# Kernel optimization log

Measured on AMD Instinct MI355X. Metric: run time of the kernel, lower is better.

Reference implementation:

```python
import jax, jax.numpy as jnp
import numpy as np

B, K, I, H = 128, 512, 512, 512  # batch, seq_len, input_dim, hidden_dim


def setup_inputs() -> dict:
    key = jax.random.key(0)
    k1, k2, k3, k4, k5 = jax.random.split(key, 5)
    s_i = 1.0 / np.sqrt(H)
    return {
        "visual_seq": jax.random.normal(k1, (B, K, I), dtype=jnp.float32),
        # PyTorch GRU layout: gates stacked [r, z, n] along first dim
        "W_ih": jax.random.uniform(k2, (3 * H, I), minval=-s_i, maxval=s_i, dtype=jnp.float32),
        "W_hh": jax.random.uniform(k3, (3 * H, H), minval=-s_i, maxval=s_i, dtype=jnp.float32),
        "b_ih": jax.random.uniform(k4, (3 * H,), minval=-s_i, maxval=s_i, dtype=jnp.float32),
        "b_hh": jax.random.uniform(k5, (3 * H,), minval=-s_i, maxval=s_i, dtype=jnp.float32),
    }


def reference(visual_seq, W_ih, W_hh, b_ih, b_hh):
    # Fused single-layer GRU over all K steps (equivalent to the per-frame
    # torch loop with zero-initialized hidden state).
    Bs, Ks, _ = visual_seq.shape
    Hs = W_hh.shape[1]
    # Precompute input-gate projections for all timesteps: (K, B, 3H)
    x_gates = jnp.einsum('bki,gi->kbg', visual_seq, W_ih) + b_ih

    def step(h, xg):
        hg = h @ W_hh.T + b_hh                      # (B, 3H)
        xr, xz, xn = jnp.split(xg, 3, axis=-1)
        hr, hz, hn = jnp.split(hg, 3, axis=-1)
        r = jax.nn.sigmoid(xr + hr)
        z = jax.nn.sigmoid(xz + hz)
        n = jnp.tanh(xn + r * hn)
        h_new = (1.0 - z) * n + z * h
        return h_new, None

    h0 = jnp.zeros((Bs, Hs), dtype=visual_seq.dtype)
    h_final, _ = jax.lax.scan(step, h0, x_gates)
    return h_final  # (B, H) == h[-1] in the torch code
```

## Files before the change

kernel.cpp:

```cpp
#include <hip/hip_runtime.h>
#include <hip/hip_bf16.h>


#define CH 32
#define XG_BYTES (CH * 128 * 1536 * 4)
#define HB_BYTES (2 * 128 * 512 * 2)
#define HSTATE_BYTES (128 * 512 * 4)
#define CNT_STRIDE 16
#define CNT_BYTES (512 * 4 * CNT_STRIDE * 4)

typedef float  floatx4 __attribute__((ext_vector_type(4)));
typedef short  shortx8 __attribute__((ext_vector_type(8)));

__device__ __forceinline__ unsigned short f2bf(float f) {
    unsigned int u = __float_as_uint(f);
    u = (u + 0x7FFFu + ((u >> 16) & 1u)) >> 16;
    return (unsigned short)u;
}

__global__ __launch_bounds__(256, 1)
void gru_fused(const float* __restrict__ vis, const float* __restrict__ Wih,
               const float* __restrict__ bih, const float* __restrict__ Whh,
               const float* __restrict__ bhh,
               const float* __restrict__ xgR, float* __restrict__ xgW,
               unsigned short* __restrict__ hb, float* __restrict__ hstate,
               unsigned int* __restrict__ cnt, float* __restrict__ out,
               int kg0, int gemm_kg0, int do_rec, int do_gemm) {
    __shared__ unsigned short Ast[64][40];
    __shared__ unsigned short Bst[64][40];

    const int bx = blockIdx.x;
    const int t = threadIdx.x;
    const int wave = t >> 6, lane = t & 63, quad = lane >> 4, l16 = lane & 15;

    if (do_rec && bx < 64) {
        const int ug = bx & 15, bg = bx >> 4;
        const int u0 = ug * 32, b0 = bg * 32;
        const int mt = wave & 1, u16 = wave >> 1;
        const int b_base = b0 + mt * 16 + quad * 4;
        const int u = u0 + u16 * 16 + l16;

        shortx8 w[3][16];
        #pragma unroll
        for (int g = 0; g < 3; ++g) {
            #pragma unroll
            for (int kt = 0; kt < 16; ++kt) {
                const float* p = Whh + ((size_t)(g * 512 + u)) * 512 + kt * 32 + quad * 8;
                float4 a = *(const float4*)p;
                float4 b = *(const float4*)(p + 4);
                shortx8 v;
                v[0] = (short)f2bf(a.x); v[1] = (short)f2bf(a.y);
                v[2] = (short)f2bf(a.z); v[3] = (short)f2bf(a.w);
                v[4] = (short)f2bf(b.x); v[5] = (short)f2bf(b.y);
                v[6] = (short)f2bf(b.z); v[7] = (short)f2bf(b.w);
                w[g][kt] = v;
            }
        }
        const float bhr = bhh[u], bhz = bhh[512 + u], bhn = bhh[1024 + u];

        float hp[4];
        if (kg0 == 0) {
            hp[0] = hp[1] = hp[2] = hp[3] = 0.f;
        } else {
            #pragma unroll
            for (int reg = 0; reg < 4; ++reg) hp[reg] = hstate[(size_t)(b_base + reg) * 512 + u];
        }

        for (int s = 0; s < CH; ++s) {
            const int kg = kg0 + s;
            float xr[4], xz[4], xn[4];
            #pragma unroll
            for (int reg = 0; reg < 4; ++reg) {
                const float* xgp = xgR + ((size_t)s * 128 + b_base + reg) * 1536 + u;
                xr[reg] = xgp[0]; xz[reg] = xgp[512]; xn[reg] = xgp[1024];
            }

            union { unsigned long long u8[2]; shortx8 v; } af[16];
            if (kg > 0) {
                const unsigned int* fp = cnt + ((size_t)(kg - 1) * 4 + bg) * CNT_STRIDE;
                while (__hip_atomic_load(fp, __ATOMIC_RELAXED, __HIP_MEMORY_SCOPE_AGENT) < 16u)
                    __builtin_amdgcn_s_sleep(1);
                const unsigned short* hsrc = hb + (size_t)((kg - 1) & 1) * (128 * 512)
                                                + (size_t)(b0 + mt * 16 + l16) * 512 + quad * 8;
                #pragma unroll
                for (int kt = 0; kt < 16; ++kt) {
                    af[kt].u8[0] = __hip_atomic_load((const unsigned long long*)(hsrc + kt * 32),
                                                     __ATOMIC_RELAXED, __HIP_MEMORY_SCOPE_AGENT);
                    af[kt].u8[1] = __hip_atomic_load((const unsigned long long*)(hsrc + kt * 32 + 4),
                                                     __ATOMIC_RELAXED, __HIP_MEMORY_SCOPE_AGENT);
                }
            } else {
                #pragma unroll
                for (int kt = 0; kt < 16; ++kt) { af[kt].u8[0] = 0ull; af[kt].u8[1] = 0ull; }
            }

            floatx4 aR = {0,0,0,0}, aZ = {0,0,0,0}, aN = {0,0,0,0};
            #pragma unroll
            for (int kt = 0; kt < 16; ++kt) {
                aR = __builtin_amdgcn_mfma_f32_16x16x32_bf16(af[kt].v, w[0][kt], aR, 0, 0, 0);
                aZ = __builtin_amdgcn_mfma_f32_16x16x32_bf16(af[kt].v, w[1][kt], aZ, 0, 0, 0);
                aN = __builtin_amdgcn_mfma_f32_16x16x32_bf16(af[kt].v, w[2][kt], aN, 0, 0, 0);
            }

            unsigned short* hdst = hb + (size_t)(kg & 1) * (128 * 512);
            #pragma unroll
            for (int reg = 0; reg < 4; ++reg) {
                const float r = 1.f / (1.f + __expf(-(xr[reg] + aR[reg] + bhr)));
                const float z = 1.f / (1.f + __expf(-(xz[reg] + aZ[reg] + bhz)));
                const float n = tanhf(xn[reg] + r * (aN[reg] + bhn));
                const float h = (1.f - z) * n + z * hp[reg];
                hp[reg] = h;
                const float h_odd = __shfl_xor(h, 1);
                if (!(lane & 1)) {
                    unsigned int pk = (unsigned int)f2bf(h) | ((unsigned int)f2bf(h_odd) << 16);
                    __hip_atomic_store((unsigned int*)(hdst + (size_t)(b_base + reg) * 512 + u),
                                       pk, __ATOMIC_RELAXED, __HIP_MEMORY_SCOPE_AGENT);
                }
                if (kg == 511) out[(size_t)(b_base + reg) * 512 + u] = h;
            }
            __syncthreads();
            if (t == 0)
                __hip_atomic_fetch_add(cnt + ((size_t)kg * 4 + bg) * CNT_STRIDE, 1u,
                                       __ATOMIC_RELAXED, __HIP_MEMORY_SCOPE_AGENT);
        }

        #pragma unroll
        for (int reg = 0; reg < 4; ++reg)
            hstate[(size_t)(b_base + reg) * 512 + u] = hp[reg];
        return;
    }

    if (!do_gemm) return;
    const int NG = do_rec ? 192 : 256;
    const int gid = do_rec ? bx - 64 : bx;

    for (int T = gid; T < 1536; T += NG) {
        const int g0 = (T % 24) * 64;
        const int m0 = (T / 24) * 64;
        const int kc = m0 >> 7;
        const int b0 = m0 & 127;
        const int kg = gemm_kg0 + kc;

        floatx4 acc[4] = {{0,0,0,0},{0,0,0,0},{0,0,0,0},{0,0,0,0}};

        for (int ki = 0; ki < 16; ++ki) {
            const int i0 = ki * 32;
            #pragma unroll
            for (int rep = 0; rep < 2; ++rep) {
                const int r = (t >> 3) + rep * 32;
                const int c = (t & 7) * 4;
                float4 av = *(const float4*)(vis + ((size_t)(b0 + r) * 512 + kg) * 512 + i0 + c);
                ushort4 ab; ab.x = f2bf(av.x); ab.y = f2bf(av.y); ab.z = f2bf(av.z); ab.w = f2bf(av.w);
                *(ushort4*)&Ast[r][c] = ab;
                float4 bv = *(const float4*)(Wih + (size_t)(g0 + r) * 512 + i0 + c);
                ushort4 bb; bb.x = f2bf(bv.x); bb.y = f2bf(bv.y); bb.z = f2bf(bv.z); bb.w = f2bf(bv.w);
                *(ushort4*)&Bst[r][c] = bb;
            }
            __syncthreads();
            shortx8 afr = *(const shortx8*)(&Ast[wave * 16 + l16][quad * 8]);
            #pragma unroll
            for (int nb = 0; nb < 4; ++nb) {
                shortx8 bfr = *(const shortx8*)(&Bst[nb * 16 + l16][quad * 8]);
                acc[nb] = __builtin_amdgcn_mfma_f32_16x16x32_bf16(afr, bfr, acc[nb], 0, 0, 0);
            }
            __syncthreads();
        }
        #pragma unroll
        for (int nb = 0; nb < 4; ++nb) {
            const int g = g0 + nb * 16 + l16;
            const float bi = bih[g];
            #pragma unroll
            for (int reg = 0; reg < 4; ++reg) {
                const int m = m0 + wave * 16 + quad * 4 + reg;
                xgW[(size_t)m * 1536 + g] = acc[nb][reg] + bi;
            }
        }
    }
}

extern "C" void kernel_launch(void* const* d_in, const int* in_sizes, int n_in,
                              void* d_out, int out_size, void* d_ws, size_t ws_size,
                              hipStream_t stream) {
    const float* vis = (const float*)d_in[0];
    const float* Wih = (const float*)d_in[1];
    const float* Whh = (const float*)d_in[2];
    const float* bih = (const float*)d_in[3];
    const float* bhh = (const float*)d_in[4];
    float* out = (float*)d_out;

    char* ws = (char*)d_ws;
    float* xg0 = (float*)ws;
    float* xg1 = (float*)(ws + XG_BYTES);
    unsigned short* hb = (unsigned short*)(ws + 2 * XG_BYTES);
    float* hstate = (float*)(ws + 2 * XG_BYTES + HB_BYTES);
    unsigned int* cnt = (unsigned int*)(ws + 2 * XG_BYTES + HB_BYTES + HSTATE_BYTES);

    hipMemsetAsync(cnt, 0, CNT_BYTES, stream);

    float* bufs[2] = {xg0, xg1};

    gru_fused<<<256, 256, 0, stream>>>(vis, Wih, bih, Whh, bhh,
                                       xg0, xg0, hb, hstate, cnt, out,
                                       0, 0, 0, 1);
    for (int i = 0; i < 16; ++i) {
        gru_fused<<<256, 256, 0, stream>>>(vis, Wih, bih, Whh, bhh,
                                           bufs[i & 1], bufs[(i + 1) & 1],
                                           hb, hstate, cnt, out,
                                           i * CH, (i + 1) * CH, 1, (i < 15) ? 1 : 0);
    }
}
```

Measured before the change: 3.657 ms.

## Replace per-step block barrier and counter with per-wave monotonic flags

Each wave now publishes its progress by storing a step number into its own flag instead of the block doing __syncthreads plus a shared atomic counter increment. Consumers poll the 32 relevant producer flags across lanes and use a ballot to wait until all have reached the current step. The recurrent-state loads become inline dwordx4 loads with sc0 sc1 cache bits in place of paired 64-bit atomic loads. The aim is to cut the block-wide barrier and atomic contention from the serial recurrence critical path. In exchange, correctness now depends on the hand-written waitcnt before each flag store for ordering, and the flag memory layout and initialisation change.

Result: faster. 3.046 ms (-16.7%).

```diff
diff --git a/kernel.cpp b/kernel.cpp
--- a/kernel.cpp
+++ b/kernel.cpp
@@ -66,6 +66,11 @@
             for (int reg = 0; reg < 4; ++reg) hp[reg] = hstate[(size_t)(b_base + reg) * 512 + u];
         }
 
+        unsigned int* const myflag =
+            cnt + ((size_t)((bg * 2 + mt) * 32 + (ug * 2 + u16))) * CNT_STRIDE;
+        const unsigned int* const pollflag =
+            cnt + ((size_t)((bg * 2 + mt) * 32 + (lane & 31))) * CNT_STRIDE;
+
         for (int s = 0; s < CH; ++s) {
             const int kg = kg0 + s;
             float xr[4], xz[4], xn[4];
@@ -77,18 +82,23 @@
 
             union { unsigned long long u8[2]; shortx8 v; } af[16];
             if (kg > 0) {
-                const unsigned int* fp = cnt + ((size_t)(kg - 1) * 4 + bg) * CNT_STRIDE;
-                while (__hip_atomic_load(fp, __ATOMIC_RELAXED, __HIP_MEMORY_SCOPE_AGENT) < 16u)
+                for (;;) {
+                    unsigned int v = __hip_atomic_load(pollflag, __ATOMIC_RELAXED,
+                                                       __HIP_MEMORY_SCOPE_AGENT);
+                    if (__ballot(v < (unsigned int)kg) == 0ull) break;
                     __builtin_amdgcn_s_sleep(1);
+                }
                 const unsigned short* hsrc = hb + (size_t)((kg - 1) & 1) * (128 * 512)
                                                 + (size_t)(b0 + mt * 16 + l16) * 512 + quad * 8;
                 #pragma unroll
                 for (int kt = 0; kt < 16; ++kt) {
-                    af[kt].u8[0] = __hip_atomic_load((const unsigned long long*)(hsrc + kt * 32),
-                                                     __ATOMIC_RELAXED, __HIP_MEMORY_SCOPE_AGENT);
-                    af[kt].u8[1] = __hip_atomic_load((const unsigned long long*)(hsrc + kt * 32 + 4),
-                                                     __ATOMIC_RELAXED, __HIP_MEMORY_SCOPE_AGENT);
+                    asm volatile("global_load_dwordx4 %0, %1, off sc0 sc1"
+                                 : "=v"(af[kt].v)
+                                 : "v"(hsrc + kt * 32)
+                                 : "memory");
                 }
+                asm volatile("s_waitcnt vmcnt(0)" ::: "memory");
+                __builtin_amdgcn_sched_barrier(0);
             } else {
                 #pragma unroll
                 for (int kt = 0; kt < 16; ++kt) { af[kt].u8[0] = 0ull; af[kt].u8[1] = 0ull; }
@@ -118,10 +128,11 @@
                 }
                 if (kg == 511) out[(size_t)(b_base + reg) * 512 + u] = h;
             }
-            __syncthreads();
-            if (t == 0)
-                __hip_atomic_fetch_add(cnt + ((size_t)kg * 4 + bg) * CNT_STRIDE, 1u,
-                                       __ATOMIC_RELAXED, __HIP_MEMORY_SCOPE_AGENT);
+            asm volatile("s_waitcnt vmcnt(0)" ::: "memory");
+            __builtin_amdgcn_sched_barrier(0);
+            if (lane == 0)
+                __hip_atomic_store(myflag, (unsigned int)(kg + 1), __ATOMIC_RELAXED,
+                                   __HIP_MEMORY_SCOPE_AGENT);
         }
 
         #pragma unroll
```

## Replace counter-based step sync with tagged hidden-state words and split GEMM/recurrence kernels

Applied to the files above, without the earlier changes.

Each hidden-state pair is now stored together with a step tag in a 64-bit word. Consumers poll the tags directly instead of waiting on a per-step block counter that needed a __syncthreads plus an atomic add. W_hh is kept in swizzled LDS rather than registers, and tanh is computed from exp. The input-projection GEMM moves to a separate kernel that runs between recurrence chunks of 64 steps, so it no longer overlaps with the recurrence; the single xg buffer and the extra launches serialize the two phases.

Measured after the change: 4.459 ms. 21.9% more time.

```diff
diff --git a/kernel.cpp b/kernel.cpp
--- a/kernel.cpp
+++ b/kernel.cpp
@@ -1,140 +1,162 @@
 #include <hip/hip_runtime.h>
-#include <hip/hip_bf16.h>
-
-
-#define CH 32
+
+
+#define CH 64
 #define XG_BYTES (CH * 128 * 1536 * 4)
-#define HB_BYTES (2 * 128 * 512 * 2)
-#define HSTATE_BYTES (128 * 512 * 4)
-#define CNT_STRIDE 16
-#define CNT_BYTES (512 * 4 * CNT_STRIDE * 4)
+#define HBT_BYTES (2 * 128 * 256 * 8)
 
 typedef float  floatx4 __attribute__((ext_vector_type(4)));
 typedef short  shortx8 __attribute__((ext_vector_type(8)));
+typedef unsigned int uintx4 __attribute__((ext_vector_type(4)));
 
 __device__ __forceinline__ unsigned short f2bf(float f) {
-    unsigned int u = __float_as_uint(f);
-    u = (u + 0x7FFFu + ((u >> 16) & 1u)) >> 16;
-    return (unsigned short)u;
+    unsigned int uu = __float_as_uint(f);
+    uu = (uu + 0x7FFFu + ((uu >> 16) & 1u)) >> 16;
+    return (unsigned short)uu;
 }
 
 __global__ __launch_bounds__(256, 1)
-void gru_fused(const float* __restrict__ vis, const float* __restrict__ Wih,
-               const float* __restrict__ bih, const float* __restrict__ Whh,
-               const float* __restrict__ bhh,
-               const float* __restrict__ xgR, float* __restrict__ xgW,
-               unsigned short* __restrict__ hb, float* __restrict__ hstate,
-               unsigned int* __restrict__ cnt, float* __restrict__ out,
-               int kg0, int gemm_kg0, int do_rec, int do_gemm) {
+void gru_rec(const float* __restrict__ xgR, const float* __restrict__ Whh,
+             const float* __restrict__ bhh,
+             unsigned long long* __restrict__ hbt, float* __restrict__ out,
+             int kg0) {
+    __shared__ unsigned short Wl[96 * 512];
+
+    const int bx = blockIdx.x, t = threadIdx.x;
+    const int wave = t >> 6, lane = t & 63, quad = lane >> 4, l16 = lane & 15;
+    const int ug = bx & 15, bg = bx >> 4;
+    const int u0 = ug * 32, b0 = bg * 32;
+    const int mt = wave & 1, u16 = wave >> 1;
+    const int b_base = b0 + mt * 16 + quad * 4;
+    const int u = u0 + u16 * 16 + l16;
+    const int rrow = b0 + mt * 16 + l16;
+
+    for (int i = t; i < 96 * 128; i += 256) {
+        const int r = i >> 7, cq = i & 127;
+        const int g = r >> 5, lu = r & 31;
+        const float* p = Whh + ((size_t)(g * 512 + u0 + lu)) * 512 + cq * 4;
+        float4 vv = *(const float4*)p;
+        ushort4 b4;
+        b4.x = f2bf(vv.x); b4.y = f2bf(vv.y); b4.z = f2bf(vv.z); b4.w = f2bf(vv.w);
+        *(ushort4*)&Wl[r * 512 + ((cq * 4) ^ ((r & 7) << 3))] = b4;
+    }
+    __syncthreads();
+
+    const float bhr = bhh[u], bhz = bhh[512 + u], bhn = bhh[1024 + u];
+    const int rb = u16 * 16 + l16, xrw = (rb & 7) << 3;
+
+    float hp[4];
+    if (kg0 == 0) {
+        hp[0] = hp[1] = hp[2] = hp[3] = 0.f;
+    } else {
+        #pragma unroll
+        for (int reg = 0; reg < 4; ++reg) hp[reg] = out[(size_t)(b_base + reg) * 512 + u];
+    }
+
+    for (int s = 0; s < CH; ++s) {
+        const int kg = kg0 + s;
+        float xr[4], xz[4], xn[4];
+        #pragma unroll
+        for (int reg = 0; reg < 4; ++reg) {
+            const float* xgp = xgR + ((size_t)s * 128 + b_base + reg) * 1536 + u;
+            xr[reg] = xgp[0]; xz[reg] = xgp[512]; xn[reg] = xgp[1024];
+        }
+
+        union { unsigned int d[4]; shortx8 v; } af[16];
+        if (kg > 0) {
+            const unsigned int expv = (unsigned int)(kg - 1);
+            const size_t pbase = (size_t)((kg - 1) & 1) * 32768;
+            const unsigned long long* sp = hbt + pbase + (size_t)rrow * 256
+                                              + ((lane & 31) >> 1) * 16 + (lane & 1) * 8;
+            for (;;) {
+                unsigned int tg = (unsigned int)(__hip_atomic_load(sp, __ATOMIC_RELAXED,
+                                                 __HIP_MEMORY_SCOPE_AGENT) >> 32);
+                if (__ballot(tg != expv) == 0ull) break;
+                __builtin_amdgcn_s_sleep(1);
+            }
+            const unsigned long long* hbp = hbt + pbase + (size_t)rrow * 256 + quad * 4;
+            union { uintx4 v; unsigned int d[4]; } Tq[32];
+            for (;;) {
+                #define LDT(i, OFF) asm volatile("global_load_dwordx4 %0, %1, off offset:" OFF " sc0 sc1" \
+                        : "=v"(Tq[i].v) : "v"(hbp) : "memory");
+                LDT(0,"0")     LDT(1,"16")    LDT(2,"128")   LDT(3,"144")
+                LDT(4,"256")   LDT(5,"272")   LDT(6,"384")   LDT(7,"400")
+                LDT(8,"512")   LDT(9,"528")   LDT(10,"640")  LDT(11,"656")
+                LDT(12,"768")  LDT(13,"784")  LDT(14,"896")  LDT(15,"912")
+                LDT(16,"1024") LDT(17,"1040") LDT(18,"1152") LDT(19,"1168")
+                LDT(20,"1280") LDT(21,"1296") LDT(22,"1408") LDT(23,"1424")
+                LDT(24,"1536") LDT(25,"1552") LDT(26,"1664") LDT(27,"1680")
+                LDT(28,"1792") LDT(29,"1808") LDT(30,"1920") LDT(31,"1936")
+                #undef LDT
+                asm volatile("s_waitcnt vmcnt(0)" ::: "memory");
+                __builtin_amdgcn_sched_barrier(0);
+                unsigned int err = 0u;
+                #pragma unroll
+                for (int i = 0; i < 32; ++i)
+                    err |= (Tq[i].d[1] ^ expv) | (Tq[i].d[3] ^ expv);
+                if (__ballot(err != 0u) == 0ull) break;
+                __builtin_amdgcn_s_sleep(1);
+            }
+            #pragma unroll
+            for (int kt = 0; kt < 16; ++kt) {
+                af[kt].d[0] = Tq[2 * kt].d[0];     af[kt].d[1] = Tq[2 * kt].d[2];
+                af[kt].d[2] = Tq[2 * kt + 1].d[0]; af[kt].d[3] = Tq[2 * kt + 1].d[2];
+            }
+        } else {
+            #pragma unroll
+            for (int kt = 0; kt < 16; ++kt) {
+                af[kt].d[0] = 0u; af[kt].d[1] = 0u; af[kt].d[2] = 0u; af[kt].d[3] = 0u;
+            }
+        }
+
+        floatx4 aR = {0,0,0,0}, aZ = {0,0,0,0}, aN = {0,0,0,0};
+        #pragma unroll
+        for (int kt = 0; kt < 16; ++kt) {
+            const int co = (kt * 32 + quad * 8) ^ xrw;
+            shortx8 bR = *(const shortx8*)&Wl[(size_t)rb * 512 + co];
+            shortx8 bZ = *(const shortx8*)&Wl[(size_t)(32 + rb) * 512 + co];
+            shortx8 bN = *(const shortx8*)&Wl[(size_t)(64 + rb) * 512 + co];
+            aR = __builtin_amdgcn_mfma_f32_16x16x32_bf16(af[kt].v, bR, aR, 0, 0, 0);
+            aZ = __builtin_amdgcn_mfma_f32_16x16x32_bf16(af[kt].v, bZ, aZ, 0, 0, 0);
+            aN = __builtin_amdgcn_mfma_f32_16x16x32_bf16(af[kt].v, bN, aN, 0, 0, 0);
+        }
+
+        unsigned long long* hdst = hbt + (size_t)(kg & 1) * 32768;
+        const unsigned long long tagv = ((unsigned long long)(unsigned int)kg) << 32;
+        #pragma unroll
+        for (int reg = 0; reg < 4; ++reg) {
+            const float r = 1.f / (1.f + __expf(-(xr[reg] + aR[reg] + bhr)));
+            const float z = 1.f / (1.f + __expf(-(xz[reg] + aZ[reg] + bhz)));
+            const float nv = xn[reg] + r * (aN[reg] + bhn);
+            const float n = 1.f - 2.f / (__expf(2.f * nv) + 1.f);
+            const float h = (1.f - z) * n + z * hp[reg];
+            hp[reg] = h;
+            const float h_odd = __shfl_xor(h, 1);
+            if (!(lane & 1)) {
+                unsigned long long val = tagv |
+                    (unsigned long long)((unsigned int)f2bf(h) |
+                                         ((unsigned int)f2bf(h_odd) << 16));
+                __hip_atomic_store(hdst + (size_t)(b_base + reg) * 256 + (u >> 1), val,
+                                   __ATOMIC_RELAXED, __HIP_MEMORY_SCOPE_AGENT);
+            }
+        }
+    }
+
+    #pragma unroll
+    for (int reg = 0; reg < 4; ++reg)
+        out[(size_t)(b_base + reg) * 512 + u] = hp[reg];
+}
+
+__global__ __launch_bounds__(256)
+void gemm_xg(const float* __restrict__ vis, const float* __restrict__ Wih,
+             const float* __restrict__ bih, float* __restrict__ xgW, int gemm_kg0) {
     __shared__ unsigned short Ast[64][40];
     __shared__ unsigned short Bst[64][40];
 
-    const int bx = blockIdx.x;
     const int t = threadIdx.x;
     const int wave = t >> 6, lane = t & 63, quad = lane >> 4, l16 = lane & 15;
 
-    if (do_rec && bx < 64) {
-        const int ug = bx & 15, bg = bx >> 4;
-        const int u0 = ug * 32, b0 = bg * 32;
-        const int mt = wave & 1, u16 = wave >> 1;
-        const int b_base = b0 + mt * 16 + quad * 4;
-        const int u = u0 + u16 * 16 + l16;
-
-        shortx8 w[3][16];
-        #pragma unroll
-        for (int g = 0; g < 3; ++g) {
-            #pragma unroll
-            for (int kt = 0; kt < 16; ++kt) {
-                const float* p = Whh + ((size_t)(g * 512 + u)) * 512 + kt * 32 + quad * 8;
-                float4 a = *(const float4*)p;
-                float4 b = *(const float4*)(p + 4);
-                shortx8 v;
-                v[0] = (short)f2bf(a.x); v[1] = (short)f2bf(a.y);
-                v[2] = (short)f2bf(a.z); v[3] = (short)f2bf(a.w);
-                v[4] = (short)f2bf(b.x); v[5] = (short)f2bf(b.y);
-                v[6] = (short)f2bf(b.z); v[7] = (short)f2bf(b.w);
-                w[g][kt] = v;
-            }
-        }
-        const float bhr = bhh[u], bhz = bhh[512 + u], bhn = bhh[1024 + u];
-
-        float hp[4];
-        if (kg0 == 0) {
-            hp[0] = hp[1] = hp[2] = hp[3] = 0.f;
-        } else {
-            #pragma unroll
-            for (int reg = 0; reg < 4; ++reg) hp[reg] = hstate[(size_t)(b_base + reg) * 512 + u];
-        }
-
-        for (int s = 0; s < CH; ++s) {
-            const int kg = kg0 + s;
-            float xr[4], xz[4], xn[4];
-            #pragma unroll
-            for (int reg = 0; reg < 4; ++reg) {
-                const float* xgp = xgR + ((size_t)s * 128 + b_base + reg) * 1536 + u;
-                xr[reg] = xgp[0]; xz[reg] = xgp[512]; xn[reg] = xgp[1024];
-            }
-
-            union { unsigned long long u8[2]; shortx8 v; } af[16];
-            if (kg > 0) {
-                const unsigned int* fp = cnt + ((size_t)(kg - 1) * 4 + bg) * CNT_STRIDE;
-                while (__hip_atomic_load(fp, __ATOMIC_RELAXED, __HIP_MEMORY_SCOPE_AGENT) < 16u)
-                    __builtin_amdgcn_s_sleep(1);
-                const unsigned short* hsrc = hb + (size_t)((kg - 1) & 1) * (128 * 512)
-                                                + (size_t)(b0 + mt * 16 + l16) * 512 + quad * 8;
-                #pragma unroll
-                for (int kt = 0; kt < 16; ++kt) {
-                    af[kt].u8[0] = __hip_atomic_load((const unsigned long long*)(hsrc + kt * 32),
-                                                     __ATOMIC_RELAXED, __HIP_MEMORY_SCOPE_AGENT);
-                    af[kt].u8[1] = __hip_atomic_load((const unsigned long long*)(hsrc + kt * 32 + 4),
-                                                     __ATOMIC_RELAXED, __HIP_MEMORY_SCOPE_AGENT);
-                }
-            } else {
-                #pragma unroll
-                for (int kt = 0; kt < 16; ++kt) { af[kt].u8[0] = 0ull; af[kt].u8[1] = 0ull; }
-            }
-
-            floatx4 aR = {0,0,0,0}, aZ = {0,0,0,0}, aN = {0,0,0,0};
-            #pragma unroll
-            for (int kt = 0; kt < 16; ++kt) {
-                aR = __builtin_amdgcn_mfma_f32_16x16x32_bf16(af[kt].v, w[0][kt], aR, 0, 0, 0);
-                aZ = __builtin_amdgcn_mfma_f32_16x16x32_bf16(af[kt].v, w[1][kt], aZ, 0, 0, 0);
-                aN = __builtin_amdgcn_mfma_f32_16x16x32_bf16(af[kt].v, w[2][kt], aN, 0, 0, 0);
-            }
-
-            unsigned short* hdst = hb + (size_t)(kg & 1) * (128 * 512);
-            #pragma unroll
-            for (int reg = 0; reg < 4; ++reg) {
-                const float r = 1.f / (1.f + __expf(-(xr[reg] + aR[reg] + bhr)));
-                const float z = 1.f / (1.f + __expf(-(xz[reg] + aZ[reg] + bhz)));
-                const float n = tanhf(xn[reg] + r * (aN[reg] + bhn));
-                const float h = (1.f - z) * n + z * hp[reg];
-                hp[reg] = h;
-                const float h_odd = __shfl_xor(h, 1);
-                if (!(lane & 1)) {
-                    unsigned int pk = (unsigned int)f2bf(h) | ((unsigned int)f2bf(h_odd) << 16);
-                    __hip_atomic_store((unsigned int*)(hdst + (size_t)(b_base + reg) * 512 + u),
-                                       pk, __ATOMIC_RELAXED, __HIP_MEMORY_SCOPE_AGENT);
-                }
-                if (kg == 511) out[(size_t)(b_base + reg) * 512 + u] = h;
-            }
-            __syncthreads();
-            if (t == 0)
-                __hip_atomic_fetch_add(cnt + ((size_t)kg * 4 + bg) * CNT_STRIDE, 1u,
-                                       __ATOMIC_RELAXED, __HIP_MEMORY_SCOPE_AGENT);
-        }
-
-        #pragma unroll
-        for (int reg = 0; reg < 4; ++reg)
-            hstate[(size_t)(b_base + reg) * 512 + u] = hp[reg];
-        return;
-    }
-
-    if (!do_gemm) return;
-    const int NG = do_rec ? 192 : 256;
-    const int gid = do_rec ? bx - 64 : bx;
-
-    for (int T = gid; T < 1536; T += NG) {
+    for (int T = blockIdx.x; T < 24 * 128; T += gridDim.x) {
         const int g0 = (T % 24) * 64;
         const int m0 = (T / 24) * 64;
         const int kc = m0 >> 7;
@@ -189,23 +211,15 @@
     float* out = (float*)d_out;
 
     char* ws = (char*)d_ws;
-    float* xg0 = (float*)ws;
-    float* xg1 = (float*)(ws + XG_BYTES);
-    unsigned short* hb = (unsigned short*)(ws + 2 * XG_BYTES);
-    float* hstate = (float*)(ws + 2 * XG_BYTES + HB_BYTES);
-    unsigned int* cnt = (unsigned int*)(ws + 2 * XG_BYTES + HB_BYTES + HSTATE_BYTES);
-
-    hipMemsetAsync(cnt, 0, CNT_BYTES, stream);
-
-    float* bufs[2] = {xg0, xg1};
-
-    gru_fused<<<256, 256, 0, stream>>>(vis, Wih, bih, Whh, bhh,
-                                       xg0, xg0, hb, hstate, cnt, out,
-                                       0, 0, 0, 1);
-    for (int i = 0; i < 16; ++i) {
-        gru_fused<<<256, 256, 0, stream>>>(vis, Wih, bih, Whh, bhh,
-                                           bufs[i & 1], bufs[(i + 1) & 1],
-                                           hb, hstate, cnt, out,
-                                           i * CH, (i + 1) * CH, 1, (i < 15) ? 1 : 0);
-    }
-}
+    float* xg = (float*)ws;
+    unsigned long long* hbt = (unsigned long long*)(ws + XG_BYTES);
+
+    hipMemsetAsync(hbt, 0xFF, HBT_BYTES, stream);
+
+    gemm_xg<<<1536, 256, 0, stream>>>(vis, Wih, bih, xg, 0);
+    for (int c = 0; c < 8; ++c) {
+        gru_rec<<<64, 256, 0, stream>>>(xg, Whh, bhh, hbt, out, c * CH);
+        if (c < 7)
+            gemm_xg<<<1536, 256, 0, stream>>>(vis, Wih, bih, xg, (c + 1) * CH);
+    }
+}
```
